# Performance work log

Hardware: AMD Instinct MI355X
Metric: run time of the kernel (lower is better)

## Reference

```python
import jax, jax.numpy as jnp
from jax import lax
import numpy as np

BETA = 0.9
THR1 = 1.0
THR2 = 0.8


def setup_inputs() -> dict:
    key = jax.random.key(0)
    ks = jax.random.split(key, 10)
    B, T, I, H, O = 256, 100, 1024, 2048, 1024
    x = jax.random.uniform(ks[0], (B, T, I), dtype=jnp.float32)
    cd1 = jax.random.normal(ks[1], (I,), dtype=jnp.float32) * 0.01
    v1 = jnp.array([0.5], dtype=jnp.float32)
    cd2 = jax.random.normal(ks[2], (H,), dtype=jnp.float32) * 0.01
    v2 = jnp.array([0.5], dtype=jnp.float32)
    W1 = jax.random.normal(ks[3], (H, I), dtype=jnp.float32) * 0.02
    b1 = jnp.zeros((H,), dtype=jnp.float32)
    W2 = jax.random.normal(ks[4], (O, H), dtype=jnp.float32) * 0.02
    b2 = jnp.zeros((O,), dtype=jnp.float32)
    out_scale = jnp.ones((O,), dtype=jnp.float32)
    out_bias = jnp.zeros((O,), dtype=jnp.float32)
    return {"x": x, "cd1": cd1, "v1": v1, "cd2": cd2, "v2": v2,
            "W1": W1, "b1": b1, "W2": W2, "b2": b2,
            "out_scale": out_scale, "out_bias": out_bias}


def _lif(inp, pot, cd, v, thr):
    # relativistic delay-weighted LIF step; inp/pot: [B, N]
    vc = jnp.clip(v, 0.0, 0.999)[0]
    gamma = 1.0 / jnp.sqrt(1.0 - vc * vc)
    delay_factors = jnp.exp(-(gamma * jnp.abs(cd) * vc))  # [N]
    new_pot = pot * BETA + inp * delay_factors
    spk = (new_pot > thr).astype(inp.dtype)
    return spk, new_pot * (1.0 - spk)


def reference(x, cd1, v1, cd2, v2, W1, b1, W2, b2, out_scale, out_bias):
    B, T, I = x.shape
    H = cd2.shape[0]
    xt = jnp.swapaxes(x, 0, 1)  # [T, B, I]

    def step(carry, x_t):
        p1, p2 = carry
        s1, p1 = _lif(x_t, p1, cd1, v1, THR1)
        h = s1 @ W1.T + b1  # [B, H]
        s2, p2 = _lif(h, p2, cd2, v2, THR2)
        o = s2 @ W2.T + b2  # [B, O]
        return (p1, p2), o

    init = (jnp.zeros((B, I), x.dtype), jnp.zeros((B, H), x.dtype))
    _, outs = lax.scan(step, init, xt)  # [T, B, O]

    vc = jnp.clip(v1, 0.0, 0.999)[0]
    gamma = 1.0 / jnp.sqrt(1.0 - vc * vc)
    t = jnp.arange(T, dtype=x.dtype)
    tw = jnp.exp(-(gamma - 1.0) * t)
    tw = tw / tw.sum()
    weighted = jnp.einsum('tbo,t->bo', outs, tw)
    return weighted * out_scale + out_bias
```

## Files before the change

kernel.cpp:

```cpp
#include <hip/hip_runtime.h>
#include <hip/hip_bf16.h>
#include <math.h>

#define BETA_F 0.9f
#define THR1_F 1.0f
#define THR2_F 0.8f

typedef __attribute__((ext_vector_type(8))) short bf16x8;
typedef __attribute__((ext_vector_type(4))) float f32x4;

__device__ __forceinline__ void gload_lds16(const void* g, void* l) {
    __builtin_amdgcn_global_load_lds(
        (const __attribute__((address_space(1))) void*)g,
        (__attribute__((address_space(3))) void*)l, 16, 0, 0);
}

__device__ __forceinline__ ushort f2bf(float f) {
    __hip_bfloat16 h = __float2bfloat16(f);
    return *(ushort*)&h;
}
__device__ __forceinline__ float bf2f(ushort u) {
    __hip_bfloat16 h;
    *(ushort*)&h = u;
    return __bfloat162float(h);
}

__global__ void k_init(const float* __restrict__ cd1, const float* __restrict__ v1,
                       const float* __restrict__ cd2, const float* __restrict__ v2,
                       float* __restrict__ df1, float* __restrict__ df2,
                       float* __restrict__ p1, float* __restrict__ p2,
                       float* __restrict__ acc2,
                       int I, int H, int BI, int BH) {
    float vc1 = fminf(fmaxf(v1[0], 0.0f), 0.999f);
    float vc2 = fminf(fmaxf(v2[0], 0.0f), 0.999f);
    double g1 = 1.0 / sqrt(1.0 - (double)vc1 * (double)vc1);
    double g2 = 1.0 / sqrt(1.0 - (double)vc2 * (double)vc2);
    int total = I + H + BI + BH + BH;
    for (int idx = blockIdx.x * blockDim.x + threadIdx.x; idx < total;
         idx += gridDim.x * blockDim.x) {
        if (idx < I) {
            df1[idx] = (float)exp(-(g1 * fabs((double)cd1[idx]) * (double)vc1));
        } else if (idx < I + H) {
            int j = idx - I;
            df2[j] = (float)exp(-(g2 * fabs((double)cd2[j]) * (double)vc2));
        } else if (idx < I + H + BI) {
            p1[idx - I - H] = 0.0f;
        } else if (idx < I + H + BI + BH) {
            p2[idx - I - H - BI] = 0.0f;
        } else {
            acc2[idx - I - H - BI - BH] = 0.0f;
        }
    }
}

__global__ void k_tw(const float* __restrict__ v1, float* __restrict__ tw, int T) {
    __shared__ float sh[256];
    float vc = fminf(fmaxf(v1[0], 0.0f), 0.999f);
    double g = 1.0 / sqrt(1.0 - (double)vc * (double)vc);
    int t = threadIdx.x;
    float val = 0.0f;
    if (t < T) val = (float)exp(-(g - 1.0) * (double)t);
    sh[t] = val;
    __syncthreads();
    for (int s = 128; s > 0; s >>= 1) {
        if (t < s) sh[t] += sh[t + s];
        __syncthreads();
    }
    float sum = sh[0];
    if (t < T) tw[t] = val / sum;
}

__global__ void k_wsplit(const float* __restrict__ W, ushort* __restrict__ hi,
                         ushort* __restrict__ lo, int n) {
    int i = blockIdx.x * blockDim.x + threadIdx.x;
    if (i >= n) return;
    float w = W[i];
    ushort h = f2bf(w);
    float hf = bf2f(h);
    ushort l = f2bf(w - hf);
    hi[i] = h;
    lo[i] = l;
}

__global__ void k_lif1(const float* __restrict__ x, const float* __restrict__ df1,
                       float* __restrict__ p1, ushort* __restrict__ s1,
                       int Bsz, int T, int I, int t0, int TC) {
    int idx = blockIdx.x * blockDim.x + threadIdx.x;
    if (idx >= Bsz * I) return;
    int b = idx / I;
    int i = idx - b * I;
    float df = df1[i];
    float p = p1[idx];
    const float* xp = x + ((size_t)b * T + t0) * I + i;
    size_t strideS = (size_t)Bsz * I;
    for (int t = 0; t < TC; ++t) {
        float xv = xp[(size_t)t * I];
        float pn = __fadd_rn(__fmul_rn(p, BETA_F), __fmul_rn(xv, df));
        bool spk = pn > THR1_F;
        s1[(size_t)t * strideS + idx] = spk ? (ushort)0x3F80 : (ushort)0;
        p = spk ? 0.0f : pn;
    }
    p1[idx] = p;
}

__global__ void k_lif2(const float* __restrict__ h, const float* __restrict__ df2,
                       const float* __restrict__ tw, float* __restrict__ p2,
                       float* __restrict__ acc2, int Bsz, int H, int t0, int TC) {
    int idx = blockIdx.x * blockDim.x + threadIdx.x;
    if (idx >= Bsz * H) return;
    int j = idx % H;
    float df = df2[j];
    float p = p2[idx];
    float acc = acc2[idx];
    size_t strideH = (size_t)Bsz * H;
    for (int t = 0; t < TC; ++t) {
        float hv = h[(size_t)t * strideH + idx];
        float pn = __fadd_rn(__fmul_rn(p, BETA_F), __fmul_rn(hv, df));
        bool spk = pn > THR2_F;
        if (spk) acc += tw[t0 + t];
        p = spk ? 0.0f : pn;
    }
    p2[idx] = p;
    acc2[idx] = acc;
}

__global__ __launch_bounds__(512, 4)
void k_gemm_mfma(const ushort* __restrict__ A, const ushort* __restrict__ Bhi,
                 const ushort* __restrict__ Blo, const float* __restrict__ bias,
                 float* __restrict__ C, int N, int K, int gx) {
    __shared__ ushort As[2][8192];
    __shared__ ushort Bh[2][4096];
    __shared__ ushort Bl[2][4096];
    int nwg = gridDim.x;
    int lin = blockIdx.x;
    int cpx = nwg >> 3;
    int swz = (lin & 7) * cpx + (lin >> 3);
    int bx = swz % gx, by = swz / gx;
    int mBase = by * 256, nBase = bx * 128;
    int tid = threadIdx.x;
    int wid = tid >> 6, lane = tid & 63;

    int srow = tid >> 2;
    int schunk = (tid & 3) ^ ((tid >> 3) & 3);
    const ushort* aS0 = A + (size_t)(mBase + srow) * K + schunk * 8;
    const ushort* aS1 = A + (size_t)(mBase + 128 + srow) * K + schunk * 8;
    const ushort* bhS = Bhi + (size_t)(nBase + srow) * K + schunk * 8;
    const ushort* blS = Blo + (size_t)(nBase + srow) * K + schunk * 8;

    int wr = wid >> 1, wc = wid & 1;
    int l15 = lane & 15;
    int sw = (l15 >> 1) & 3;
    int ch = ((lane >> 4) ^ sw) * 8;
    int aoff = (wr * 64 + l15) * 32 + ch;
    int boff = (wc * 64 + l15) * 32 + ch;

    f32x4 acc[4][4];
#pragma unroll
    for (int i = 0; i < 4; i++)
#pragma unroll
        for (int j = 0; j < 4; j++) acc[i][j] = (f32x4)(0.0f);

    auto stage = [&](int buf, int k0) {
        gload_lds16(aS0 + k0, &As[buf][tid * 8]);
        gload_lds16(aS1 + k0, &As[buf][4096 + tid * 8]);
        gload_lds16(bhS + k0, &Bh[buf][tid * 8]);
        gload_lds16(blS + k0, &Bl[buf][tid * 8]);
    };
    auto compute_tile = [&](int cur) {
        bf16x8 af[4], bf[4];
#pragma unroll
        for (int f = 0; f < 4; f++) af[f] = *(const bf16x8*)&As[cur][aoff + f * 512];
#pragma unroll
        for (int f = 0; f < 4; f++) bf[f] = *(const bf16x8*)&Bh[cur][boff + f * 512];
        __builtin_amdgcn_s_setprio(1);
#pragma unroll
        for (int i = 0; i < 4; i++)
#pragma unroll
            for (int j = 0; j < 4; j++)
                acc[i][j] = __builtin_amdgcn_mfma_f32_16x16x32_bf16(af[i], bf[j],
                                                                    acc[i][j], 0, 0, 0);
        __builtin_amdgcn_s_setprio(0);
#pragma unroll
        for (int f = 0; f < 4; f++) bf[f] = *(const bf16x8*)&Bl[cur][boff + f * 512];
        __builtin_amdgcn_s_setprio(1);
#pragma unroll
        for (int i = 0; i < 4; i++)
#pragma unroll
            for (int j = 0; j < 4; j++)
                acc[i][j] = __builtin_amdgcn_mfma_f32_16x16x32_bf16(af[i], bf[j],
                                                                    acc[i][j], 0, 0, 0);
        __builtin_amdgcn_s_setprio(0);
    };

    int NT = K >> 5;
    stage(0, 0);
    __syncthreads();
    for (int kt = 0; kt < NT - 1; ++kt) {
        stage((kt + 1) & 1, (kt + 1) << 5);
        compute_tile(kt & 1);
        __syncthreads();
    }
    compute_tile((NT - 1) & 1);

    int crow0 = mBase + wr * 64 + (lane >> 4) * 4;
    int ccol0 = nBase + wc * 64 + l15;
#pragma unroll
    for (int i = 0; i < 4; i++) {
#pragma unroll
        for (int j = 0; j < 4; j++) {
            int col = ccol0 + j * 16;
            float bv = bias[col];
#pragma unroll
            for (int r = 0; r < 4; r++) {
                int row = crow0 + i * 16 + r;
                C[(size_t)row * N + col] = acc[i][j][r] + bv;
            }
        }
    }
}

__global__ __launch_bounds__(256)
void k_gemm64(const float* __restrict__ A, const float* __restrict__ Bm,
              float* __restrict__ P, int M, int N, int K, int KS) {
    __shared__ float As[16][68];
    __shared__ float Bs[16][68];
    int tid = threadIdx.x;
    int mBase = blockIdx.y * 64, nBase = blockIdx.x * 64;
    int k0 = blockIdx.z * KS;
    int lr = tid >> 2, lk = (tid & 3) * 4;
    int ty = tid >> 4, tx = tid & 15;
    float acc[4][4];
#pragma unroll
    for (int i = 0; i < 4; i++)
#pragma unroll
        for (int j = 0; j < 4; j++) acc[i][j] = 0.0f;
    const float* Ap = A + (size_t)(mBase + lr) * K + k0 + lk;
    const float* Bp = Bm + (size_t)(nBase + lr) * K + k0 + lk;
    for (int k = 0; k < KS; k += 16) {
        float4 av = *(const float4*)(Ap + k);
        float4 bv = *(const float4*)(Bp + k);
        __syncthreads();
        As[lk + 0][lr] = av.x; As[lk + 1][lr] = av.y;
        As[lk + 2][lr] = av.z; As[lk + 3][lr] = av.w;
        Bs[lk + 0][lr] = bv.x; Bs[lk + 1][lr] = bv.y;
        Bs[lk + 2][lr] = bv.z; Bs[lk + 3][lr] = bv.w;
        __syncthreads();
#pragma unroll
        for (int kk = 0; kk < 16; ++kk) {
            float4 a4 = *(const float4*)&As[kk][ty * 4];
            float4 b4 = *(const float4*)&Bs[kk][tx * 4];
            float aa[4] = {a4.x, a4.y, a4.z, a4.w};
            float bb[4] = {b4.x, b4.y, b4.z, b4.w};
#pragma unroll
            for (int i = 0; i < 4; i++)
#pragma unroll
                for (int j = 0; j < 4; j++)
                    acc[i][j] = fmaf(aa[i], bb[j], acc[i][j]);
        }
    }
#pragma unroll
    for (int i = 0; i < 4; i++)
#pragma unroll
        for (int j = 0; j < 4; j++)
            P[((size_t)blockIdx.z * M + mBase + ty * 4 + i) * N + nBase + tx * 4 + j] =
                acc[i][j];
}

__global__ void k_fin(const float* __restrict__ P, const float* __restrict__ b2,
                      const float* __restrict__ scale, const float* __restrict__ bias2,
                      float* __restrict__ out, int M, int N, int Z) {
    int i = blockIdx.x * blockDim.x + threadIdx.x;
    if (i >= M * N) return;
    float s = 0.0f;
    for (int z = 0; z < Z; ++z) s += P[(size_t)z * M * N + i];
    int col = i % N;
    out[i] = (s + b2[col]) * scale[col] + bias2[col];
}

extern "C" void kernel_launch(void* const* d_in, const int* in_sizes, int n_in,
                              void* d_out, int out_size, void* d_ws, size_t ws_size,
                              hipStream_t stream) {
    const float* x = (const float*)d_in[0];
    const float* cd1 = (const float*)d_in[1];
    const float* v1 = (const float*)d_in[2];
    const float* cd2 = (const float*)d_in[3];
    const float* v2 = (const float*)d_in[4];
    const float* W1 = (const float*)d_in[5];
    const float* b1 = (const float*)d_in[6];
    const float* W2 = (const float*)d_in[7];
    const float* b2 = (const float*)d_in[8];
    const float* out_scale = (const float*)d_in[9];
    const float* out_bias = (const float*)d_in[10];

    int I = in_sizes[1];
    int H = in_sizes[3];
    int O = in_sizes[8];
    int Bsz = out_size / O;
    int T = in_sizes[0] / (Bsz * I);
    const int ZSPLIT = 4;

    float* ws = (float*)d_ws;
    size_t off = 0;
    auto alloc = [&](size_t n) {
        size_t cur = off;
        off += (n + 63) & ~(size_t)63;
        return cur;
    };
    size_t o_df1 = alloc(I);
    size_t o_df2 = alloc(H);
    size_t o_tw = alloc(T);
    size_t o_p1 = alloc((size_t)Bsz * I);
    size_t o_p2 = alloc((size_t)Bsz * H);
    size_t o_acc2 = alloc((size_t)Bsz * H);
    size_t o_whi = alloc((size_t)H * I / 2);
    size_t o_wlo = alloc((size_t)H * I / 2);
    size_t o_part = alloc((size_t)ZSPLIT * Bsz * O);
    size_t persist = off;

    size_t wsFloats = ws_size / 4;
    size_t perStep = (size_t)Bsz * I / 2 + (size_t)Bsz * H + 128;
    int TC = 1;
    if (wsFloats > persist) {
        size_t tcMax = (wsFloats - persist) / perStep;
        TC = (int)(tcMax < (size_t)T ? tcMax : (size_t)T);
        if (TC < 1) TC = 1;
    }
    size_t o_s1 = alloc(((size_t)TC * Bsz * I + 1) / 2);
    size_t o_h = alloc((size_t)TC * Bsz * H);

    float* df1 = ws + o_df1;
    float* df2 = ws + o_df2;
    float* tw = ws + o_tw;
    float* p1 = ws + o_p1;
    float* p2 = ws + o_p2;
    float* acc2 = ws + o_acc2;
    ushort* whi = (ushort*)(ws + o_whi);
    ushort* wlo = (ushort*)(ws + o_wlo);
    float* part = ws + o_part;
    ushort* s1c = (ushort*)(ws + o_s1);
    float* hbuf = ws + o_h;

    k_init<<<2048, 256, 0, stream>>>(cd1, v1, cd2, v2, df1, df2, p1, p2, acc2, I, H,
                                     Bsz * I, Bsz * H);
    k_tw<<<1, 256, 0, stream>>>(v1, tw, T);
    k_wsplit<<<(H * I + 255) / 256, 256, 0, stream>>>(W1, whi, wlo, H * I);

    for (int t0 = 0; t0 < T; t0 += TC) {
        int tc = (T - t0 < TC) ? (T - t0) : TC;
        k_lif1<<<(Bsz * I + 255) / 256, 256, 0, stream>>>(x, df1, p1, s1c, Bsz, T, I,
                                                          t0, tc);
        int Mrows = tc * Bsz;
        int gx = H / 128;
        int nwg = (Mrows / 256) * gx;
        k_gemm_mfma<<<nwg, 512, 0, stream>>>(s1c, whi, wlo, b1, hbuf, H, I, gx);
        k_lif2<<<(Bsz * H + 255) / 256, 256, 0, stream>>>(hbuf, df2, tw, p2, acc2,
                                                          Bsz, H, t0, tc);
    }
    dim3 g2(O / 64, Bsz / 64, ZSPLIT);
    k_gemm64<<<g2, 256, 0, stream>>>(acc2, W2, part, Bsz, O, H, H / ZSPLIT);
    k_fin<<<(Bsz * O + 255) / 256, 256, 0, stream>>>(part, b2, out_scale, out_bias,
                                                     (float*)d_out, Bsz, O, ZSPLIT);
}
```

Baseline: 518.5 us.

## Concatenate W1 hi/lo along K and enlarge MFMA GEMM tile to 256x256

```diff
diff --git a/kernel.cpp b/kernel.cpp
--- a/kernel.cpp
+++ b/kernel.cpp
@@ -70,16 +70,17 @@
     if (t < T) tw[t] = val / sum;
 }
 
-__global__ void k_wsplit(const float* __restrict__ W, ushort* __restrict__ hi,
-                         ushort* __restrict__ lo, int n) {
+__global__ void k_wsplit(const float* __restrict__ W, ushort* __restrict__ bcat,
+                         int n, int I) {
     int i = blockIdx.x * blockDim.x + threadIdx.x;
     if (i >= n) return;
     float w = W[i];
     ushort h = f2bf(w);
     float hf = bf2f(h);
     ushort l = f2bf(w - hf);
-    hi[i] = h;
-    lo[i] = l;
+    int row = i / I, k = i - row * I;
+    bcat[(size_t)row * 2 * I + k] = h;
+    bcat[(size_t)row * 2 * I + I + k] = l;
 }
 
 __global__ void k_lif1(const float* __restrict__ x, const float* __restrict__ df1,
@@ -124,96 +125,113 @@
     acc2[idx] = acc;
 }
 
-__global__ __launch_bounds__(512, 4)
-void k_gemm_mfma(const ushort* __restrict__ A, const ushort* __restrict__ Bhi,
-                 const ushort* __restrict__ Blo, const float* __restrict__ bias,
-                 float* __restrict__ C, int N, int K, int gx) {
-    __shared__ ushort As[2][8192];
-    __shared__ ushort Bh[2][4096];
-    __shared__ ushort Bl[2][4096];
+__global__ __launch_bounds__(512, 2)
+void k_gemm_mfma(const ushort* __restrict__ A, const ushort* __restrict__ Bc,
+                 const float* __restrict__ bias, float* __restrict__ C,
+                 int N, int K1, int gx) {
+    __shared__ ushort As[2][16384];
+    __shared__ ushort Bs[2][16384];
     int nwg = gridDim.x;
     int lin = blockIdx.x;
     int cpx = nwg >> 3;
     int swz = (lin & 7) * cpx + (lin >> 3);
     int bx = swz % gx, by = swz / gx;
-    int mBase = by * 256, nBase = bx * 128;
+    int mBase = by * 256, nBase = bx * 256;
     int tid = threadIdx.x;
     int wid = tid >> 6, lane = tid & 63;
-
-    int srow = tid >> 2;
-    int schunk = (tid & 3) ^ ((tid >> 3) & 3);
-    const ushort* aS0 = A + (size_t)(mBase + srow) * K + schunk * 8;
-    const ushort* aS1 = A + (size_t)(mBase + 128 + srow) * K + schunk * 8;
-    const ushort* bhS = Bhi + (size_t)(nBase + srow) * K + schunk * 8;
-    const ushort* blS = Blo + (size_t)(nBase + srow) * K + schunk * 8;
-
-    int wr = wid >> 1, wc = wid & 1;
-    int l15 = lane & 15;
-    int sw = (l15 >> 1) & 3;
-    int ch = ((lane >> 4) ^ sw) * 8;
-    int aoff = (wr * 64 + l15) * 32 + ch;
-    int boff = (wc * 64 + l15) * 32 + ch;
-
-    f32x4 acc[4][4];
-#pragma unroll
-    for (int i = 0; i < 4; i++)
-#pragma unroll
-        for (int j = 0; j < 4; j++) acc[i][j] = (f32x4)(0.0f);
-
-    auto stage = [&](int buf, int k0) {
-        gload_lds16(aS0 + k0, &As[buf][tid * 8]);
-        gload_lds16(aS1 + k0, &As[buf][4096 + tid * 8]);
-        gload_lds16(bhS + k0, &Bh[buf][tid * 8]);
-        gload_lds16(blS + k0, &Bl[buf][tid * 8]);
+    int K2 = 2 * K1;
+
+    int srow = tid >> 3;
+    int p = tid & 7;
+    int lch = (p ^ (srow & 7)) * 8;
+    const ushort* aSeg[4];
+    const ushort* bSeg[4];
+#pragma unroll
+    for (int s = 0; s < 4; s++) {
+        aSeg[s] = A + (size_t)(mBase + s * 64 + srow) * K1 + lch;
+        bSeg[s] = Bc + (size_t)(nBase + s * 64 + srow) * K2 + lch;
+    }
+    int ldsOff = tid * 8;
+
+    auto stage = [&](int buf, int kt) {
+        int k0 = kt << 6;
+        int aK = k0 & (K1 - 1);
+#pragma unroll
+        for (int s = 0; s < 4; s++)
+            gload_lds16(aSeg[s] + aK, &As[buf][s * 4096 + ldsOff]);
+#pragma unroll
+        for (int s = 0; s < 4; s++)
+            gload_lds16(bSeg[s] + k0, &Bs[buf][s * 4096 + ldsOff]);
     };
-    auto compute_tile = [&](int cur) {
-        bf16x8 af[4], bf[4];
-#pragma unroll
-        for (int f = 0; f < 4; f++) af[f] = *(const bf16x8*)&As[cur][aoff + f * 512];
-#pragma unroll
-        for (int f = 0; f < 4; f++) bf[f] = *(const bf16x8*)&Bh[cur][boff + f * 512];
+
+    int wr = wid >> 2, wc = wid & 3;
+    int hi = lane >> 4, l15 = lane & 15;
+    int sw7 = l15 & 7;
+    int aRow = (wr * 128 + l15) * 64;
+    int bRow = (wc * 64 + l15) * 64;
+    int aoff0 = aRow + ((hi ^ sw7) * 8);
+    int aoff1 = aRow + (((4 + hi) ^ sw7) * 8);
+    int boff0 = bRow + ((hi ^ sw7) * 8);
+    int boff1 = bRow + (((4 + hi) ^ sw7) * 8);
+
+    f32x4 acc[8][4];
+#pragma unroll
+    for (int f = 0; f < 8; f++)
+#pragma unroll
+        for (int j = 0; j < 4; j++) acc[f][j] = (f32x4)(0.0f);
+
+    auto compute = [&](int cur) {
+        bf16x8 af[8], bf[4];
+#pragma unroll
+        for (int f = 0; f < 8; f++) af[f] = *(const bf16x8*)&As[cur][aoff0 + f * 1024];
+#pragma unroll
+        for (int j = 0; j < 4; j++) bf[j] = *(const bf16x8*)&Bs[cur][boff0 + j * 1024];
         __builtin_amdgcn_s_setprio(1);
 #pragma unroll
-        for (int i = 0; i < 4; i++)
+        for (int f = 0; f < 8; f++)
 #pragma unroll
             for (int j = 0; j < 4; j++)
-                acc[i][j] = __builtin_amdgcn_mfma_f32_16x16x32_bf16(af[i], bf[j],
-                                                                    acc[i][j], 0, 0, 0);
+                acc[f][j] = __builtin_amdgcn_mfma_f32_16x16x32_bf16(af[f], bf[j],
+                                                                    acc[f][j], 0, 0, 0);
         __builtin_amdgcn_s_setprio(0);
 #pragma unroll
-        for (int f = 0; f < 4; f++) bf[f] = *(const bf16x8*)&Bl[cur][boff + f * 512];
+        for (int f = 0; f < 8; f++) af[f] = *(const bf16x8*)&As[cur][aoff1 + f * 1024];
+#pragma unroll
+        for (int j = 0; j < 4; j++) bf[j] = *(const bf16x8*)&Bs[cur][boff1 + j * 1024];
         __builtin_amdgcn_s_setprio(1);
 #pragma unroll
-        for (int i = 0; i < 4; i++)
+        for (int f = 0; f < 8; f++)
 #pragma unroll
             for (int j = 0; j < 4; j++)
-                acc[i][j] = __builtin_amdgcn_mfma_f32_16x16x32_bf16(af[i], bf[j],
-                                                                    acc[i][j], 0, 0, 0);
+                acc[f][j] = __builtin_amdgcn_mfma_f32_16x16x32_bf16(af[f], bf[j],
+                                                                    acc[f][j], 0, 0, 0);
         __builtin_amdgcn_s_setprio(0);
     };
 
-    int NT = K >> 5;
+    int NT = K2 >> 6;
     stage(0, 0);
-    __syncthreads();
+    stage(1, 1);
     for (int kt = 0; kt < NT - 1; ++kt) {
-        stage((kt + 1) & 1, (kt + 1) << 5);
-        compute_tile(kt & 1);
-        __syncthreads();
-    }
-    compute_tile((NT - 1) & 1);
-
-    int crow0 = mBase + wr * 64 + (lane >> 4) * 4;
+        asm volatile("s_waitcnt vmcnt(8)\ns_barrier" ::: "memory");
+        compute(kt & 1);
+        asm volatile("s_barrier" ::: "memory");
+        if (kt + 2 < NT) stage(kt & 1, kt + 2);
+    }
+    asm volatile("s_waitcnt vmcnt(0)\ns_barrier" ::: "memory");
+    compute((NT - 1) & 1);
+
+    int crow0 = mBase + wr * 128 + hi * 4;
     int ccol0 = nBase + wc * 64 + l15;
 #pragma unroll
-    for (int i = 0; i < 4; i++) {
+    for (int f = 0; f < 8; f++) {
 #pragma unroll
         for (int j = 0; j < 4; j++) {
             int col = ccol0 + j * 16;
             float bv = bias[col];
 #pragma unroll
             for (int r = 0; r < 4; r++) {
-                int row = crow0 + i * 16 + r;
-                C[(size_t)row * N + col] = acc[i][j][r] + bv;
+                int row = crow0 + f * 16 + r;
+                C[(size_t)row * N + col] = acc[f][j][r] + bv;
             }
         }
     }
@@ -312,8 +330,7 @@
     size_t o_p1 = alloc((size_t)Bsz * I);
     size_t o_p2 = alloc((size_t)Bsz * H);
     size_t o_acc2 = alloc((size_t)Bsz * H);
-    size_t o_whi = alloc((size_t)H * I / 2);
-    size_t o_wlo = alloc((size_t)H * I / 2);
+    size_t o_bcat = alloc((size_t)H * I);
     size_t o_part = alloc((size_t)ZSPLIT * Bsz * O);
     size_t persist = off;
 
@@ -334,8 +351,7 @@
     float* p1 = ws + o_p1;
     float* p2 = ws + o_p2;
     float* acc2 = ws + o_acc2;
-    ushort* whi = (ushort*)(ws + o_whi);
-    ushort* wlo = (ushort*)(ws + o_wlo);
+    ushort* bcat = (ushort*)(ws + o_bcat);
     float* part = ws + o_part;
     ushort* s1c = (ushort*)(ws + o_s1);
     float* hbuf = ws + o_h;
@@ -343,16 +359,16 @@
     k_init<<<2048, 256, 0, stream>>>(cd1, v1, cd2, v2, df1, df2, p1, p2, acc2, I, H,
                                      Bsz * I, Bsz * H);
     k_tw<<<1, 256, 0, stream>>>(v1, tw, T);
-    k_wsplit<<<(H * I + 255) / 256, 256, 0, stream>>>(W1, whi, wlo, H * I);
+    k_wsplit<<<(H * I + 255) / 256, 256, 0, stream>>>(W1, bcat, H * I, I);
 
     for (int t0 = 0; t0 < T; t0 += TC) {
         int tc = (T - t0 < TC) ? (T - t0) : TC;
         k_lif1<<<(Bsz * I + 255) / 256, 256, 0, stream>>>(x, df1, p1, s1c, Bsz, T, I,
                                                           t0, tc);
         int Mrows = tc * Bsz;
-        int gx = H / 128;
+        int gx = H / 256;
         int nwg = (Mrows / 256) * gx;
-        k_gemm_mfma<<<nwg, 512, 0, stream>>>(s1c, whi, wlo, b1, hbuf, H, I, gx);
+        k_gemm_mfma<<<nwg, 512, 0, stream>>>(s1c, bcat, b1, hbuf, H, I, gx);
         k_lif2<<<(Bsz * H + 255) / 256, 256, 0, stream>>>(hbuf, df2, tw, p2, acc2,
                                                           Bsz, H, t0, tc);
     }
```

Result: slower. 585.6 us (+12.9%).
